# Performance work log

Hardware: AMD Instinct MI355X
Metric: run time of the kernel (lower is better)

Reference implementation:

```python
import jax, jax.numpy as jnp
import numpy as np

H = 128
NUM_GRAPHS = 256
NUM_TASKS = 40
BN_EPS = 1e-5


def setup_inputs() -> dict:
    key = jax.random.key(0)
    ks = jax.random.split(key, 32)
    N, E, F = 50000, 600000, 9
    inp = {}
    inp["x"] = jax.random.randint(ks[0], (N, 1), 0, 2)
    inp["edge_index"] = jax.random.randint(ks[1], (2, E), 0, N)
    inp["edge_attr"] = jax.random.uniform(ks[2], (E, F), dtype=jnp.float32)
    inp["batch"] = jnp.sort(jax.random.randint(ks[3], (N,), 0, NUM_GRAPHS))
    inp["self_loop_index"] = 7
    inp["self_loop_type"] = 1
    # parameters
    s = 0.02
    inp["node_emb"] = jax.random.normal(ks[4], (2, H), jnp.float32) * s
    for l in range(2):
        o = 5 + l * 11
        inp[f"enc_w{l}"] = jax.random.normal(ks[o + 0], (F, H), jnp.float32) * s
        inp[f"enc_b{l}"] = jnp.zeros((H,), jnp.float32)
        inp[f"w1_{l}"] = jax.random.normal(ks[o + 1], (2 * H, 2 * H), jnp.float32) * s
        inp[f"b1_{l}"] = jnp.zeros((2 * H,), jnp.float32)
        inp[f"gamma{l}"] = jnp.ones((2 * H,), jnp.float32)
        inp[f"beta{l}"] = jnp.zeros((2 * H,), jnp.float32)
        inp[f"mean{l}"] = jax.random.normal(ks[o + 2], (2 * H,), jnp.float32) * 0.1
        inp[f"var{l}"] = jax.random.uniform(ks[o + 3], (2 * H,), jnp.float32, 0.5, 1.5)
        inp[f"w2_{l}"] = jax.random.normal(ks[o + 4], (2 * H, H), jnp.float32) * s
        inp[f"b2_{l}"] = jnp.zeros((H,), jnp.float32)
    inp["pred_w"] = jax.random.normal(ks[30], (2 * H, NUM_TASKS), jnp.float32) * s
    inp["pred_b"] = jnp.zeros((NUM_TASKS,), jnp.float32)
    return inp


def _gin_layer(h, ei, ea, N, enc_w, enc_b, w1, b1, gamma, beta, mean, var, w2, b2):
    # edge encode: Linear(F, H) on all (real + self-loop) edges
    e = ea @ enc_w + enc_b                                  # [E+N, H]
    msg = jnp.concatenate([h[ei[1]], e], axis=1)            # [E+N, 2H] (feature_concat)
    agg = jax.ops.segment_sum(msg, ei[0], num_segments=N)   # sum pooling -> [N, 2H]
    z = agg @ w1 + b1
    z = (z - mean) * jax.lax.rsqrt(var + BN_EPS) * gamma + beta  # BatchNorm1d (eval)
    z = jax.nn.relu(z)
    return z @ w2 + b2                                      # [N, H]


def reference(x, edge_index, edge_attr, batch, self_loop_index, self_loop_type,
              node_emb,
              enc_w0, enc_b0, w1_0, b1_0, gamma0, beta0, mean0, var0, w2_0, b2_0,
              enc_w1, enc_b1, w1_1, b1_1, gamma1, beta1, mean1, var1, w2_1, b2_1,
              pred_w, pred_b):
    N = x.shape[0]
    loop = jnp.arange(N, dtype=edge_index.dtype)
    ei = jnp.concatenate([edge_index, jnp.stack([loop, loop])], axis=1)  # add self loops
    sl_attr = jnp.zeros((N, edge_attr.shape[1]), edge_attr.dtype).at[:, self_loop_index].set(
        jnp.asarray(self_loop_type, edge_attr.dtype))
    ea = jnp.concatenate([edge_attr, sl_attr], axis=0)       # [E+N, F]

    h0 = node_emb[x.reshape(-1)]                             # input node embedding [N, H]
    h1 = jax.nn.relu(_gin_layer(h0, ei, ea, N, enc_w0, enc_b0, w1_0, b1_0,
                                gamma0, beta0, mean0, var0, w2_0, b2_0))
    h2 = _gin_layer(h1, ei, ea, N, enc_w1, enc_b1, w1_1, b1_1,
                    gamma1, beta1, mean1, var1, w2_1, b2_1)  # JK='last'

    # graph mean pooling over batch ids
    sums = jax.ops.segment_sum(h2, batch, num_segments=NUM_GRAPHS)
    cnt = jax.ops.segment_sum(jnp.ones((N,), h2.dtype), batch, num_segments=NUM_GRAPHS)
    pooled = sums / jnp.maximum(cnt, 1.0)[:, None]
    graph_rep = jnp.concatenate([pooled, pooled], axis=1)    # no center_node_idx
    return graph_rep @ pred_w + pred_b                       # [G, num_tasks]
```

## Files before the change

### kernel.cpp

```cpp
#include <hip/hip_runtime.h>

#define H   128
#define H2  256
#define NG  256
#define NT  40
#define NF  9

typedef __attribute__((ext_vector_type(8))) short short8;
typedef __attribute__((ext_vector_type(4))) float f32x4;

#define MFMA16(a, b, c) __builtin_amdgcn_mfma_f32_16x16x32_bf16(a, b, c, 0, 0, 0)

__device__ __forceinline__ void f2bf_hilo(float x, unsigned short& hi, unsigned short& lo) {
  unsigned u = __float_as_uint(x);
  unsigned hh = (u + 0x7FFFu + ((u >> 16) & 1u)) >> 16;
  float hf = __uint_as_float(hh << 16);
  float r = x - hf;
  unsigned v = __float_as_uint(r);
  unsigned ll = (v + 0x7FFFu + ((v >> 16) & 1u)) >> 16;
  hi = (unsigned short)hh;
  lo = (unsigned short)ll;
}

__device__ __forceinline__ void cvt8(float4 a, float4 b, short8& hi, short8& lo) {
  float xs[8] = {a.x, a.y, a.z, a.w, b.x, b.y, b.z, b.w};
#pragma unroll
  for (int j = 0; j < 8; j++) {
    unsigned short h, l;
    f2bf_hilo(xs[j], h, l);
    hi[j] = (short)h;
    lo[j] = (short)l;
  }
}

__global__ void k_h0(const int* __restrict__ x, const float* __restrict__ emb,
                     float* __restrict__ h, int N) {
  int i = blockIdx.x * blockDim.x + threadIdx.x;
  if (i >= N * 32) return;
  int v = i >> 5, q = i & 31;
  ((float4*)h)[i] = ((const float4*)emb)[x[v] * 32 + q];
}

__global__ void k_deg(const int* __restrict__ ei, unsigned* __restrict__ deg, int E) {
  int e = blockIdx.x * blockDim.x + threadIdx.x;
  if (e >= E) return;
  atomicAdd(&deg[ei[e]], 1u);
}

__global__ __launch_bounds__(1024) void k_scan(const unsigned* __restrict__ deg,
                                               unsigned* __restrict__ off,
                                               unsigned* __restrict__ cur, int N) {
  __shared__ unsigned wsum[16];
  __shared__ unsigned wpre[16];
  __shared__ unsigned s_run;
  int tid = threadIdx.x;
  int lane = tid & 63, wv = tid >> 6;
  if (tid == 0) s_run = 0u;
  __syncthreads();
  for (int base = 0; base < N; base += 4096) {
    int i0 = base + tid * 4;
    unsigned v0 = 0, v1 = 0, v2 = 0, v3 = 0;
    if (i0 + 0 < N) v0 = deg[i0 + 0];
    if (i0 + 1 < N) v1 = deg[i0 + 1];
    if (i0 + 2 < N) v2 = deg[i0 + 2];
    if (i0 + 3 < N) v3 = deg[i0 + 3];
    unsigned tsum = v0 + v1 + v2 + v3;
    unsigned sc = tsum;
#pragma unroll
    for (int d = 1; d < 64; d <<= 1) {
      unsigned t = __shfl_up(sc, d);
      if (lane >= d) sc += t;
    }
    if (lane == 63) wsum[wv] = sc;
    __syncthreads();
    if (wv == 0 && lane < 16) {
      unsigned xv = wsum[lane];
#pragma unroll
      for (int d = 1; d < 16; d <<= 1) {
        unsigned t = __shfl_up(xv, d);
        if (lane >= d) xv += t;
      }
      wpre[lane] = xv;
    }
    __syncthreads();
    unsigned excl = s_run + (wv ? wpre[wv - 1] : 0u) + (sc - tsum);
    unsigned p1 = excl + v0, p2 = p1 + v1, p3 = p2 + v2;
    if (i0 + 0 < N) { off[i0 + 0] = excl; cur[i0 + 0] = excl; }
    if (i0 + 1 < N) { off[i0 + 1] = p1;   cur[i0 + 1] = p1; }
    if (i0 + 2 < N) { off[i0 + 2] = p2;   cur[i0 + 2] = p2; }
    if (i0 + 3 < N) { off[i0 + 3] = p3;   cur[i0 + 3] = p3; }
    __syncthreads();
    if (tid == 0) s_run += wpre[15];
  }
  if (tid == 0) off[N] = s_run;
}

__global__ void k_scatter(const int* __restrict__ ei, unsigned* __restrict__ cur,
                          int* __restrict__ csrc, int* __restrict__ ceid, int E) {
  int e = blockIdx.x * blockDim.x + threadIdx.x;
  if (e >= E) return;
  int dst = ei[e], src = ei[E + e];
  unsigned pos = atomicAdd(&cur[dst], 1u);
  csrc[pos] = src;
  ceid[pos] = e;
}

__global__ __launch_bounds__(256) void k_S(const float* __restrict__ ea,
    const unsigned* __restrict__ off, const int* __restrict__ ceid,
    float* __restrict__ S, int N) {
  int lane = threadIdx.x & 63;
  int wv = threadIdx.x >> 6;
  int sub = lane & 7;
  int v = blockIdx.x * 32 + wv * 8 + (lane >> 3);
  if (v >= N) return;
  unsigned o = off[v], e = off[v + 1];
  float acc[NF];
#pragma unroll
  for (int f = 0; f < NF; f++) acc[f] = 0.f;
  for (unsigned i = o + sub; i < e; i += 8) {
    const float* a = ea + (size_t)ceid[i] * NF;
#pragma unroll
    for (int f = 0; f < NF; f++) acc[f] += a[f];
  }
#pragma unroll
  for (int d = 1; d < 8; d <<= 1)
#pragma unroll
    for (int f = 0; f < NF; f++) acc[f] += __shfl_xor(acc[f], d);
  if (sub == 0) {
#pragma unroll
    for (int f = 0; f < NF; f++) S[(size_t)v * NF + f] = acc[f];
  }
}

__global__ __launch_bounds__(256) void k_gather(const float* __restrict__ h,
    const unsigned* __restrict__ off, const int* __restrict__ csrc,
    float* __restrict__ hs, int N) {
  int v = blockIdx.x * 4 + (threadIdx.x >> 6);
  int lane = threadIdx.x & 63;
  if (v >= N) return;
  unsigned o = off[v], e = off[v + 1];
  const float2* hp = (const float2*)h;
  float2 acc = hp[(size_t)v * 64 + lane];
  for (unsigned i = o; i < e; i++) {
    int s = csrc[i];
    float2 t = hp[(size_t)s * 64 + lane];
    acc.x += t.x; acc.y += t.y;
  }
  ((float2*)hs)[(size_t)v * 64 + lane] = acc;
}

__global__ void k_prepA(const float* __restrict__ enc_w, const float* __restrict__ enc_b,
                        const float* __restrict__ w1, const float* __restrict__ b1,
                        const float* __restrict__ gamma, const float* __restrict__ beta,
                        const float* __restrict__ mean, const float* __restrict__ var,
                        const int* __restrict__ sli, const int* __restrict__ slt,
                        unsigned short* __restrict__ BAhi, unsigned short* __restrict__ BAlo,
                        float* __restrict__ cc) {
  int c = threadIdx.x;
  float m[NF];
  float u = 0.f;
#pragma unroll
  for (int f = 0; f < NF; f++) m[f] = 0.f;
  for (int k = 0; k < H; k++) {
    float wv = w1[(size_t)(H + k) * H2 + c];
#pragma unroll
    for (int f = 0; f < NF; f++) m[f] += enc_w[f * H + k] * wv;
    u += enc_b[k] * wv;
  }
  float k0 = (float)(*slt) * m[*sli] + u + b1[c];
  float scv = gamma[c] * rsqrtf(var[c] + 1e-5f);
  cc[c] = scv;
  cc[H2 + c] = beta[c] - mean[c] * scv;
  int ct = c >> 4, cl = c & 15;
  for (int k = 0; k < 160; k++) {
    float val;
    if (k < 128)      val = w1[(size_t)k * H2 + c];
    else if (k < 137) val = m[k - 128];
    else if (k == 137) val = u;
    else if (k == 138) val = k0;
    else              val = 0.f;
    unsigned short h, l;
    f2bf_hilo(val, h, l);
    int ks = k >> 5, kr = k & 31;
    int lane = (kr >> 3) * 16 + cl, j = kr & 7;
    size_t idx = ((size_t)((ks * 16 + ct) * 64 + lane)) * 8 + j;
    BAhi[idx] = h;
    BAlo[idx] = l;
  }
}

__global__ void k_prepB2(const float* __restrict__ w2,
                         unsigned short* __restrict__ BBhi, unsigned short* __restrict__ BBlo) {
  int t = threadIdx.x;
  int c = t & 127, half = t >> 7;
  int ct = c >> 4, cl = c & 15;
  for (int kk = 0; kk < 128; kk++) {
    int k = half * 128 + kk;
    float val = w2[(size_t)k * H + c];
    unsigned short h, l;
    f2bf_hilo(val, h, l);
    int ks = k >> 5, kr = k & 31;
    int lane = (kr >> 3) * 16 + cl, j = kr & 7;
    size_t idx = ((size_t)((ks * 8 + ct) * 64 + lane)) * 8 + j;
    BBhi[idx] = h;
    BBlo[idx] = l;
  }
}

__global__ __launch_bounds__(256) void k_layer(
    const float* __restrict__ hs, const float* __restrict__ S,
    const unsigned* __restrict__ deg,
    const unsigned short* __restrict__ BAhi, const unsigned short* __restrict__ BAlo,
    const unsigned short* __restrict__ BBhi, const unsigned short* __restrict__ BBlo,
    const float* __restrict__ cc, const float* __restrict__ b2,
    float* __restrict__ out, const int* __restrict__ batch,
    int N, int relu_out, int pool) {
  __shared__ float ext[32][36];
  __shared__ unsigned short zhi[32 * 256];
  __shared__ unsigned short zlo[32 * 256];
  int tid = threadIdx.x;
  int row0 = blockIdx.x * 32;

  for (int i = tid; i < 32 * 36; i += 256) {
    int r = i / 36, c2 = i - r * 36;
    int v = row0 + r;
    float val = 0.f;
    if (v < N) {
      if (c2 < NF) val = S[(size_t)v * NF + c2];
      else if (c2 == 9) val = (float)deg[v];
      else if (c2 == 10) val = 1.0f;
    }
    ext[r][c2] = val;
  }
  __syncthreads();

  int l = tid & 63, wv = tid >> 6;
  int rowoff = (wv >> 1) * 16;
  int ctoffA = (wv & 1) * 8;
  int lr = l & 15, lg = l >> 4;

  f32x4 acc[8];
#pragma unroll
  for (int ct = 0; ct < 8; ct++) acc[ct] = f32x4{0.f, 0.f, 0.f, 0.f};

#pragma unroll
  for (int ks = 0; ks < 4; ks++) {
    int row = row0 + rowoff + lr;
    int rowc = row < N ? row : N - 1;
    const float* src = hs + (size_t)rowc * H + ks * 32 + lg * 8;
    float4 x0 = ((const float4*)src)[0];
    float4 x1 = ((const float4*)src)[1];
    short8 ahi, alo;
    cvt8(x0, x1, ahi, alo);
#pragma unroll
    for (int ct = 0; ct < 8; ct++) {
      int gct = ctoffA + ct;
      short8 bhi = ((const short8*)BAhi)[((ks * 16 + gct) << 6) + l];
      short8 blo = ((const short8*)BAlo)[((ks * 16 + gct) << 6) + l];
      acc[ct] = MFMA16(ahi, bhi, acc[ct]);
      acc[ct] = MFMA16(ahi, blo, acc[ct]);
      acc[ct] = MFMA16(alo, bhi, acc[ct]);
    }
  }
  {
    const float* src = &ext[rowoff + lr][lg * 8];
    float4 x0 = ((const float4*)src)[0];
    float4 x1 = ((const float4*)src)[1];
    short8 ahi, alo;
    cvt8(x0, x1, ahi, alo);
#pragma unroll
    for (int ct = 0; ct < 8; ct++) {
      int gct = ctoffA + ct;
      short8 bhi = ((const short8*)BAhi)[((4 * 16 + gct) << 6) + l];
      short8 blo = ((const short8*)BAlo)[((4 * 16 + gct) << 6) + l];
      acc[ct] = MFMA16(ahi, bhi, acc[ct]);
      acc[ct] = MFMA16(ahi, blo, acc[ct]);
      acc[ct] = MFMA16(alo, bhi, acc[ct]);
    }
  }

#pragma unroll
  for (int ct = 0; ct < 8; ct++) {
    int c = (ctoffA + ct) * 16 + lr;
    float scv = cc[c], shv = cc[H2 + c];
#pragma unroll
    for (int r = 0; r < 4; r++) {
      float z = acc[ct][r] * scv + shv;
      z = fmaxf(z, 0.f);
      unsigned short h, lo2;
      f2bf_hilo(z, h, lo2);
      int zr = rowoff + lg * 4 + r;
      unsigned off = (unsigned)(zr * 512 + c * 2) ^ (unsigned)((zr & 7) << 4);
      *(unsigned short*)((char*)zhi + off) = h;
      *(unsigned short*)((char*)zlo + off) = lo2;
    }
  }
  __syncthreads();

  f32x4 acc2[4];
#pragma unroll
  for (int ct = 0; ct < 4; ct++) acc2[ct] = f32x4{0.f, 0.f, 0.f, 0.f};
#pragma unroll
  for (int ks = 0; ks < 8; ks++) {
    int zr = rowoff + lr;
    unsigned off = (unsigned)(zr * 512 + (ks * 32 + lg * 8) * 2) ^ (unsigned)((zr & 7) << 4);
    short8 ahi = *(const short8*)((char*)zhi + off);
    short8 alo = *(const short8*)((char*)zlo + off);
#pragma unroll
    for (int ct = 0; ct < 4; ct++) {
      int gct = (wv & 1) * 4 + ct;
      short8 bhi = ((const short8*)BBhi)[((ks * 8 + gct) << 6) + l];
      short8 blo = ((const short8*)BBlo)[((ks * 8 + gct) << 6) + l];
      acc2[ct] = MFMA16(ahi, bhi, acc2[ct]);
      acc2[ct] = MFMA16(ahi, blo, acc2[ct]);
      acc2[ct] = MFMA16(alo, bhi, acc2[ct]);
    }
  }

#pragma unroll
  for (int ct = 0; ct < 4; ct++) {
    int c2 = ((wv & 1) * 4 + ct) * 16 + lr;
    float bias = b2[c2];
#pragma unroll
    for (int r = 0; r < 4; r++) {
      int row = row0 + rowoff + lg * 4 + r;
      if (row >= N) continue;
      float val = acc2[ct][r] + bias;
      if (relu_out) val = fmaxf(val, 0.f);
      if (pool) {
        atomicAdd(&out[(size_t)batch[row] * H + c2], val);
      } else {
        out[(size_t)row * H + c2] = val;
      }
    }
  }
}

__global__ void k_cnt(const int* __restrict__ batch, float* __restrict__ cnt, int N) {
  int v = blockIdx.x * blockDim.x + threadIdx.x;
  if (v < N) atomicAdd(&cnt[batch[v]], 1.0f);
}

__global__ void k_pred(const float* __restrict__ pooled, const float* __restrict__ cnt,
                       const float* __restrict__ pw, const float* __restrict__ pb,
                       float* __restrict__ outp) {
  int g = blockIdx.x;
  int t = threadIdx.x;
  if (t >= NT) return;
  float acc = 0.f;
  for (int k = 0; k < H; k++)
    acc += pooled[(size_t)g * H + k] * (pw[k * NT + t] + pw[(H + k) * NT + t]);
  float c = fmaxf(cnt[g], 1.0f);
  outp[(size_t)g * NT + t] = acc / c + pb[t];
}

extern "C" void kernel_launch(void* const* d_in, const int* in_sizes, int n_in,
                              void* d_out, int out_size, void* d_ws, size_t ws_size,
                              hipStream_t stream) {
  const int*   x     = (const int*)d_in[0];
  const int*   ei    = (const int*)d_in[1];
  const float* ea    = (const float*)d_in[2];
  const int*   batch = (const int*)d_in[3];
  const int*   sli   = (const int*)d_in[4];
  const int*   slt   = (const int*)d_in[5];
  const float* emb   = (const float*)d_in[6];
  const float* encw[2] = {(const float*)d_in[7],  (const float*)d_in[17]};
  const float* encb[2] = {(const float*)d_in[8],  (const float*)d_in[18]};
  const float* w1[2]   = {(const float*)d_in[9],  (const float*)d_in[19]};
  const float* b1[2]   = {(const float*)d_in[10], (const float*)d_in[20]};
  const float* gam[2]  = {(const float*)d_in[11], (const float*)d_in[21]};
  const float* bet[2]  = {(const float*)d_in[12], (const float*)d_in[22]};
  const float* mea[2]  = {(const float*)d_in[13], (const float*)d_in[23]};
  const float* var[2]  = {(const float*)d_in[14], (const float*)d_in[24]};
  const float* w2[2]   = {(const float*)d_in[15], (const float*)d_in[25]};
  const float* b2[2]   = {(const float*)d_in[16], (const float*)d_in[26]};
  const float* pw = (const float*)d_in[27];
  const float* pb = (const float*)d_in[28];

  int N = in_sizes[0];
  int E = in_sizes[1] / 2;

  char* p = (char*)d_ws;
  auto alloc = [&](size_t bytes) {
    char* r = p;
    p += (bytes + 255) / 256 * 256;
    return r;
  };
  unsigned* deg    = (unsigned*)alloc((size_t)N * 4);
  float*    S      = (float*)alloc((size_t)N * NF * 4);
  unsigned* off    = (unsigned*)alloc((size_t)(N + 1) * 4);
  unsigned* cur    = (unsigned*)alloc((size_t)N * 4);
  int*      csrc   = (int*)alloc((size_t)E * 4);
  int*      ceid   = (int*)alloc((size_t)E * 4);
  float*    hA     = (float*)alloc((size_t)N * H * 4);
  float*    hS     = (float*)alloc((size_t)N * H * 4);
  float*    hB     = (float*)alloc((size_t)N * H * 4);
  unsigned short* BAhi = (unsigned short*)alloc((size_t)5 * 16 * 64 * 8 * 2);
  unsigned short* BAlo = (unsigned short*)alloc((size_t)5 * 16 * 64 * 8 * 2);
  unsigned short* BBhi = (unsigned short*)alloc((size_t)8 * 8 * 64 * 8 * 2);
  unsigned short* BBlo = (unsigned short*)alloc((size_t)8 * 8 * 64 * 8 * 2);
  float*    cc     = (float*)alloc((size_t)2 * H2 * 4);
  float*    pooled = (float*)alloc((size_t)NG * H * 4);
  float*    cnt    = (float*)alloc((size_t)NG * 4);

  hipMemsetAsync(deg, 0, (size_t)N * 4, stream);
  hipMemsetAsync(pooled, 0, (size_t)NG * H * 4, stream);
  hipMemsetAsync(cnt, 0, (size_t)NG * 4, stream);

  int nblk = (N + 31) / 32;

  k_h0<<<(N * 32 + 255) / 256, 256, 0, stream>>>(x, emb, hA, N);
  k_deg<<<(E + 255) / 256, 256, 0, stream>>>(ei, deg, E);
  k_scan<<<1, 1024, 0, stream>>>(deg, off, cur, N);
  k_scatter<<<(E + 255) / 256, 256, 0, stream>>>(ei, cur, csrc, ceid, E);
  k_S<<<(N + 31) / 32, 256, 0, stream>>>(ea, off, ceid, S, N);

  k_prepA<<<1, 256, 0, stream>>>(encw[0], encb[0], w1[0], b1[0], gam[0], bet[0],
                                 mea[0], var[0], sli, slt, BAhi, BAlo, cc);
  k_prepB2<<<1, 256, 0, stream>>>(w2[0], BBhi, BBlo);
  k_gather<<<(N + 3) / 4, 256, 0, stream>>>(hA, off, csrc, hS, N);
  k_layer<<<nblk, 256, 0, stream>>>(hS, S, deg, BAhi, BAlo, BBhi, BBlo, cc, b2[0],
                                    hB, batch, N, 1, 0);
  k_prepA<<<1, 256, 0, stream>>>(encw[1], encb[1], w1[1], b1[1], gam[1], bet[1],
                                 mea[1], var[1], sli, slt, BAhi, BAlo, cc);
  k_prepB2<<<1, 256, 0, stream>>>(w2[1], BBhi, BBlo);
  k_gather<<<(N + 3) / 4, 256, 0, stream>>>(hB, off, csrc, hS, N);
  k_layer<<<nblk, 256, 0, stream>>>(hS, S, deg, BAhi, BAlo, BBhi, BBlo, cc, b2[1],
                                    pooled, batch, N, 0, 1);

  k_cnt<<<(N + 255) / 256, 256, 0, stream>>>(batch, cnt, N);
  k_pred<<<NG, 64, 0, stream>>>(pooled, cnt, pw, pb, (float*)d_out);
}
```

Measured before the change: 827.9 us.

## Fold layer-0 embedding aggregation into per-node neighbor counts, skipping first gather

Since input node features take only two embedding values, the layer-0 neighbor sum is rewritten as counts of neighbors with x=0 and x=1, packed into the high bits of the degree atomic. The embedding is folded through W1 in the prep kernel, so layer 0 needs no h0 materialization, no gather and no 128-wide K loop; it uses a single 32-wide K slab. The gather loop is also unrolled by four with independent accumulators, and weight prep for both layers is hoisted up front into separate buffers. This relies on x being binary and degrees fitting in 16 bits.

```diff
diff --git a/kernel.cpp b/kernel.cpp
--- a/kernel.cpp
+++ b/kernel.cpp
@@ -33,21 +33,15 @@
   }
 }
 
-__global__ void k_h0(const int* __restrict__ x, const float* __restrict__ emb,
-                     float* __restrict__ h, int N) {
-  int i = blockIdx.x * blockDim.x + threadIdx.x;
-  if (i >= N * 32) return;
-  int v = i >> 5, q = i & 31;
-  ((float4*)h)[i] = ((const float4*)emb)[x[v] * 32 + q];
-}
-
-__global__ void k_deg(const int* __restrict__ ei, unsigned* __restrict__ deg, int E) {
+__global__ void k_degc(const int* __restrict__ ei, const int* __restrict__ x,
+                       unsigned* __restrict__ degc, int E) {
   int e = blockIdx.x * blockDim.x + threadIdx.x;
   if (e >= E) return;
-  atomicAdd(&deg[ei[e]], 1u);
-}
-
-__global__ __launch_bounds__(1024) void k_scan(const unsigned* __restrict__ deg,
+  int dst = ei[e], src = ei[E + e];
+  atomicAdd(&degc[dst], 1u + ((unsigned)x[src] << 16));
+}
+
+__global__ __launch_bounds__(1024) void k_scan(const unsigned* __restrict__ degc,
                                                unsigned* __restrict__ off,
                                                unsigned* __restrict__ cur, int N) {
   __shared__ unsigned wsum[16];
@@ -60,10 +54,10 @@
   for (int base = 0; base < N; base += 4096) {
     int i0 = base + tid * 4;
     unsigned v0 = 0, v1 = 0, v2 = 0, v3 = 0;
-    if (i0 + 0 < N) v0 = deg[i0 + 0];
-    if (i0 + 1 < N) v1 = deg[i0 + 1];
-    if (i0 + 2 < N) v2 = deg[i0 + 2];
-    if (i0 + 3 < N) v3 = deg[i0 + 3];
+    if (i0 + 0 < N) v0 = degc[i0 + 0] & 0xFFFFu;
+    if (i0 + 1 < N) v1 = degc[i0 + 1] & 0xFFFFu;
+    if (i0 + 2 < N) v2 = degc[i0 + 2] & 0xFFFFu;
+    if (i0 + 3 < N) v3 = degc[i0 + 3] & 0xFFFFu;
     unsigned tsum = v0 + v1 + v2 + v3;
     unsigned sc = tsum;
 #pragma unroll
@@ -141,21 +135,79 @@
   unsigned o = off[v], e = off[v + 1];
   const float2* hp = (const float2*)h;
   float2 acc = hp[(size_t)v * 64 + lane];
-  for (unsigned i = o; i < e; i++) {
-    int s = csrc[i];
-    float2 t = hp[(size_t)s * 64 + lane];
+  float2 a0 = {0.f, 0.f}, a1 = {0.f, 0.f}, a2 = {0.f, 0.f}, a3 = {0.f, 0.f};
+  unsigned i = o;
+  for (; i + 4 <= e; i += 4) {
+    int s0 = csrc[i], s1 = csrc[i + 1], s2 = csrc[i + 2], s3 = csrc[i + 3];
+    float2 t0 = hp[(size_t)s0 * 64 + lane];
+    float2 t1 = hp[(size_t)s1 * 64 + lane];
+    float2 t2 = hp[(size_t)s2 * 64 + lane];
+    float2 t3 = hp[(size_t)s3 * 64 + lane];
+    a0.x += t0.x; a0.y += t0.y;
+    a1.x += t1.x; a1.y += t1.y;
+    a2.x += t2.x; a2.y += t2.y;
+    a3.x += t3.x; a3.y += t3.y;
+  }
+  for (; i < e; i++) {
+    float2 t = hp[(size_t)csrc[i] * 64 + lane];
     acc.x += t.x; acc.y += t.y;
   }
+  acc.x += (a0.x + a1.x) + (a2.x + a3.x);
+  acc.y += (a0.y + a1.y) + (a2.y + a3.y);
   ((float2*)hs)[(size_t)v * 64 + lane] = acc;
 }
 
-__global__ void k_prepA(const float* __restrict__ enc_w, const float* __restrict__ enc_b,
-                        const float* __restrict__ w1, const float* __restrict__ b1,
-                        const float* __restrict__ gamma, const float* __restrict__ beta,
-                        const float* __restrict__ mean, const float* __restrict__ var,
-                        const int* __restrict__ sli, const int* __restrict__ slt,
-                        unsigned short* __restrict__ BAhi, unsigned short* __restrict__ BAlo,
-                        float* __restrict__ cc) {
+__global__ void k_prepA0(const float* __restrict__ emb,
+                         const float* __restrict__ enc_w, const float* __restrict__ enc_b,
+                         const float* __restrict__ w1, const float* __restrict__ b1,
+                         const float* __restrict__ gamma, const float* __restrict__ beta,
+                         const float* __restrict__ mean, const float* __restrict__ var,
+                         const int* __restrict__ sli, const int* __restrict__ slt,
+                         unsigned short* __restrict__ BAhi, unsigned short* __restrict__ BAlo,
+                         float* __restrict__ cc) {
+  int c = threadIdx.x;
+  float e0 = 0.f, e1 = 0.f, u = 0.f;
+  float m[NF];
+#pragma unroll
+  for (int f = 0; f < NF; f++) m[f] = 0.f;
+  for (int k = 0; k < H; k++) {
+    float wt = w1[(size_t)k * H2 + c];
+    e0 += emb[k] * wt;
+    e1 += emb[H + k] * wt;
+    float wb = w1[(size_t)(H + k) * H2 + c];
+#pragma unroll
+    for (int f = 0; f < NF; f++) m[f] += enc_w[f * H + k] * wb;
+    u += enc_b[k] * wb;
+  }
+  float k0 = (float)(*slt) * m[*sli] + u + b1[c];
+  float scv = gamma[c] * rsqrtf(var[c] + 1e-5f);
+  cc[c] = scv;
+  cc[H2 + c] = beta[c] - mean[c] * scv;
+  int ct = c >> 4, cl = c & 15;
+  for (int k = 0; k < 32; k++) {
+    float val;
+    if (k == 0)       val = e0;
+    else if (k == 1)  val = e1;
+    else if (k < 11)  val = m[k - 2];
+    else if (k == 11) val = u;
+    else if (k == 12) val = k0;
+    else              val = 0.f;
+    unsigned short h, l;
+    f2bf_hilo(val, h, l);
+    int lane = (k >> 3) * 16 + cl, j = k & 7;
+    size_t idx = ((size_t)(ct * 64 + lane)) * 8 + j;
+    BAhi[idx] = h;
+    BAlo[idx] = l;
+  }
+}
+
+__global__ void k_prepA1(const float* __restrict__ enc_w, const float* __restrict__ enc_b,
+                         const float* __restrict__ w1, const float* __restrict__ b1,
+                         const float* __restrict__ gamma, const float* __restrict__ beta,
+                         const float* __restrict__ mean, const float* __restrict__ var,
+                         const int* __restrict__ sli, const int* __restrict__ slt,
+                         unsigned short* __restrict__ BAhi, unsigned short* __restrict__ BAlo,
+                         float* __restrict__ cc) {
   int c = threadIdx.x;
   float m[NF];
   float u = 0.f;
@@ -209,12 +261,12 @@
 
 __global__ __launch_bounds__(256) void k_layer(
     const float* __restrict__ hs, const float* __restrict__ S,
-    const unsigned* __restrict__ deg,
+    const unsigned* __restrict__ degc, const int* __restrict__ x,
     const unsigned short* __restrict__ BAhi, const unsigned short* __restrict__ BAlo,
     const unsigned short* __restrict__ BBhi, const unsigned short* __restrict__ BBlo,
     const float* __restrict__ cc, const float* __restrict__ b2,
     float* __restrict__ out, const int* __restrict__ batch,
-    int N, int relu_out, int pool) {
+    int N, int relu_out, int pool, int nks) {
   __shared__ float ext[32][36];
   __shared__ unsigned short zhi[32 * 256];
   __shared__ unsigned short zlo[32 * 256];
@@ -226,9 +278,20 @@
     int v = row0 + r;
     float val = 0.f;
     if (v < N) {
-      if (c2 < NF) val = S[(size_t)v * NF + c2];
-      else if (c2 == 9) val = (float)deg[v];
-      else if (c2 == 10) val = 1.0f;
+      unsigned pk = degc[v];
+      float dg = (float)(pk & 0xFFFFu);
+      float c1 = (float)(pk >> 16);
+      if (nks == 0) {
+        if (c2 == 0)       val = (dg - c1) + ((x[v] == 0) ? 1.f : 0.f);
+        else if (c2 == 1)  val = c1 + ((x[v] != 0) ? 1.f : 0.f);
+        else if (c2 < 11)  val = S[(size_t)v * NF + (c2 - 2)];
+        else if (c2 == 11) val = dg;
+        else if (c2 == 12) val = 1.0f;
+      } else {
+        if (c2 < NF)       val = S[(size_t)v * NF + c2];
+        else if (c2 == 9)  val = dg;
+        else if (c2 == 10) val = 1.0f;
+      }
     }
     ext[r][c2] = val;
   }
@@ -243,23 +306,25 @@
 #pragma unroll
   for (int ct = 0; ct < 8; ct++) acc[ct] = f32x4{0.f, 0.f, 0.f, 0.f};
 
-#pragma unroll
-  for (int ks = 0; ks < 4; ks++) {
-    int row = row0 + rowoff + lr;
-    int rowc = row < N ? row : N - 1;
-    const float* src = hs + (size_t)rowc * H + ks * 32 + lg * 8;
-    float4 x0 = ((const float4*)src)[0];
-    float4 x1 = ((const float4*)src)[1];
-    short8 ahi, alo;
-    cvt8(x0, x1, ahi, alo);
-#pragma unroll
-    for (int ct = 0; ct < 8; ct++) {
-      int gct = ctoffA + ct;
-      short8 bhi = ((const short8*)BAhi)[((ks * 16 + gct) << 6) + l];
-      short8 blo = ((const short8*)BAlo)[((ks * 16 + gct) << 6) + l];
-      acc[ct] = MFMA16(ahi, bhi, acc[ct]);
-      acc[ct] = MFMA16(ahi, blo, acc[ct]);
-      acc[ct] = MFMA16(alo, bhi, acc[ct]);
+  if (nks) {
+#pragma unroll
+    for (int ks = 0; ks < 4; ks++) {
+      int row = row0 + rowoff + lr;
+      int rowc = row < N ? row : N - 1;
+      const float* src = hs + (size_t)rowc * H + ks * 32 + lg * 8;
+      float4 x0 = ((const float4*)src)[0];
+      float4 x1 = ((const float4*)src)[1];
+      short8 ahi, alo;
+      cvt8(x0, x1, ahi, alo);
+#pragma unroll
+      for (int ct = 0; ct < 8; ct++) {
+        int gct = ctoffA + ct;
+        short8 bhi = ((const short8*)BAhi)[((ks * 16 + gct) << 6) + l];
+        short8 blo = ((const short8*)BAlo)[((ks * 16 + gct) << 6) + l];
+        acc[ct] = MFMA16(ahi, bhi, acc[ct]);
+        acc[ct] = MFMA16(ahi, blo, acc[ct]);
+        acc[ct] = MFMA16(alo, bhi, acc[ct]);
+      }
     }
   }
   {
@@ -271,8 +336,8 @@
 #pragma unroll
     for (int ct = 0; ct < 8; ct++) {
       int gct = ctoffA + ct;
-      short8 bhi = ((const short8*)BAhi)[((4 * 16 + gct) << 6) + l];
-      short8 blo = ((const short8*)BAlo)[((4 * 16 + gct) << 6) + l];
+      short8 bhi = ((const short8*)BAhi)[((nks * 16 + gct) << 6) + l];
+      short8 blo = ((const short8*)BAlo)[((nks * 16 + gct) << 6) + l];
       acc[ct] = MFMA16(ahi, bhi, acc[ct]);
       acc[ct] = MFMA16(ahi, blo, acc[ct]);
       acc[ct] = MFMA16(alo, bhi, acc[ct]);
@@ -386,47 +451,50 @@
     p += (bytes + 255) / 256 * 256;
     return r;
   };
-  unsigned* deg    = (unsigned*)alloc((size_t)N * 4);
+  unsigned* degc   = (unsigned*)alloc((size_t)N * 4);
   float*    S      = (float*)alloc((size_t)N * NF * 4);
   unsigned* off    = (unsigned*)alloc((size_t)(N + 1) * 4);
   unsigned* cur    = (unsigned*)alloc((size_t)N * 4);
   int*      csrc   = (int*)alloc((size_t)E * 4);
   int*      ceid   = (int*)alloc((size_t)E * 4);
-  float*    hA     = (float*)alloc((size_t)N * H * 4);
+  float*    hB     = (float*)alloc((size_t)N * H * 4);
   float*    hS     = (float*)alloc((size_t)N * H * 4);
-  float*    hB     = (float*)alloc((size_t)N * H * 4);
-  unsigned short* BAhi = (unsigned short*)alloc((size_t)5 * 16 * 64 * 8 * 2);
-  unsigned short* BAlo = (unsigned short*)alloc((size_t)5 * 16 * 64 * 8 * 2);
-  unsigned short* BBhi = (unsigned short*)alloc((size_t)8 * 8 * 64 * 8 * 2);
-  unsigned short* BBlo = (unsigned short*)alloc((size_t)8 * 8 * 64 * 8 * 2);
-  float*    cc     = (float*)alloc((size_t)2 * H2 * 4);
+  unsigned short* BA0hi = (unsigned short*)alloc((size_t)16 * 64 * 8 * 2);
+  unsigned short* BA0lo = (unsigned short*)alloc((size_t)16 * 64 * 8 * 2);
+  unsigned short* BA1hi = (unsigned short*)alloc((size_t)5 * 16 * 64 * 8 * 2);
+  unsigned short* BA1lo = (unsigned short*)alloc((size_t)5 * 16 * 64 * 8 * 2);
+  unsigned short* BB0hi = (unsigned short*)alloc((size_t)8 * 8 * 64 * 8 * 2);
+  unsigned short* BB0lo = (unsigned short*)alloc((size_t)8 * 8 * 64 * 8 * 2);
+  unsigned short* BB1hi = (unsigned short*)alloc((size_t)8 * 8 * 64 * 8 * 2);
+  unsigned short* BB1lo = (unsigned short*)alloc((size_t)8 * 8 * 64 * 8 * 2);
+  float*    cc0    = (float*)alloc((size_t)2 * H2 * 4);
+  float*    cc1    = (float*)alloc((size_t)2 * H2 * 4);
   float*    pooled = (float*)alloc((size_t)NG * H * 4);
   float*    cnt    = (float*)alloc((size_t)NG * 4);
 
-  hipMemsetAsync(deg, 0, (size_t)N * 4, stream);
+  hipMemsetAsync(degc, 0, (size_t)N * 4, stream);
   hipMemsetAsync(pooled, 0, (size_t)NG * H * 4, stream);
   hipMemsetAsync(cnt, 0, (size_t)NG * 4, stream);
 
   int nblk = (N + 31) / 32;
 
-  k_h0<<<(N * 32 + 255) / 256, 256, 0, stream>>>(x, emb, hA, N);
-  k_deg<<<(E + 255) / 256, 256, 0, stream>>>(ei, deg, E);
-  k_scan<<<1, 1024, 0, stream>>>(deg, off, cur, N);
+  k_degc<<<(E + 255) / 256, 256, 0, stream>>>(ei, x, degc, E);
+  k_scan<<<1, 1024, 0, stream>>>(degc, off, cur, N);
   k_scatter<<<(E + 255) / 256, 256, 0, stream>>>(ei, cur, csrc, ceid, E);
   k_S<<<(N + 31) / 32, 256, 0, stream>>>(ea, off, ceid, S, N);
 
-  k_prepA<<<1, 256, 0, stream>>>(encw[0], encb[0], w1[0], b1[0], gam[0], bet[0],
-                                 mea[0], var[0], sli, slt, BAhi, BAlo, cc);
-  k_prepB2<<<1, 256, 0, stream>>>(w2[0], BBhi, BBlo);
-  k_gather<<<(N + 3) / 4, 256, 0, stream>>>(hA, off, csrc, hS, N);
-  k_layer<<<nblk, 256, 0, stream>>>(hS, S, deg, BAhi, BAlo, BBhi, BBlo, cc, b2[0],
-                                    hB, batch, N, 1, 0);
-  k_prepA<<<1, 256, 0, stream>>>(encw[1], encb[1], w1[1], b1[1], gam[1], bet[1],
-                                 mea[1], var[1], sli, slt, BAhi, BAlo, cc);
-  k_prepB2<<<1, 256, 0, stream>>>(w2[1], BBhi, BBlo);
+  k_prepA0<<<1, 256, 0, stream>>>(emb, encw[0], encb[0], w1[0], b1[0], gam[0], bet[0],
+                                  mea[0], var[0], sli, slt, BA0hi, BA0lo, cc0);
+  k_prepB2<<<1, 256, 0, stream>>>(w2[0], BB0hi, BB0lo);
+  k_prepA1<<<1, 256, 0, stream>>>(encw[1], encb[1], w1[1], b1[1], gam[1], bet[1],
+                                  mea[1], var[1], sli, slt, BA1hi, BA1lo, cc1);
+  k_prepB2<<<1, 256, 0, stream>>>(w2[1], BB1hi, BB1lo);
+
+  k_layer<<<nblk, 256, 0, stream>>>(nullptr, S, degc, x, BA0hi, BA0lo, BB0hi, BB0lo,
+                                    cc0, b2[0], hB, batch, N, 1, 0, 0);
   k_gather<<<(N + 3) / 4, 256, 0, stream>>>(hB, off, csrc, hS, N);
-  k_layer<<<nblk, 256, 0, stream>>>(hS, S, deg, BAhi, BAlo, BBhi, BBlo, cc, b2[1],
-                                    pooled, batch, N, 0, 1);
+  k_layer<<<nblk, 256, 0, stream>>>(hS, S, degc, x, BA1hi, BA1lo, BB1hi, BB1lo,
+                                    cc1, b2[1], pooled, batch, N, 0, 1, 4);
 
   k_cnt<<<(N + 255) / 256, 256, 0, stream>>>(batch, cnt, N);
   k_pred<<<NG, 64, 0, stream>>>(pooled, cnt, pw, pb, (float*)d_out);
```

Measured after the change: 679.9 us. -17.9%, faster.
